# Kernel optimization log

Measured on AMD Instinct MI355X. Metric: run time of the kernel, lower is better.

The kernel has to match this reference:

```python
import jax, jax.numpy as jnp
import numpy as np

N_HEADS = 16
D_EMBED = 1024
N_CROSS = 768
D_HEAD = D_EMBED // N_HEADS


def setup_inputs() -> dict:
    key = jax.random.key(0)
    ks = jax.random.split(key, 10)
    B, S = 2, 2048
    x = jax.random.normal(ks[0], (B, S, D_EMBED), dtype=jnp.float32)
    context = jax.random.normal(ks[1], (B, S, N_CROSS), dtype=jnp.float32)
    sq = 1.0 / np.sqrt(D_EMBED)
    sc = 1.0 / np.sqrt(N_CROSS)
    Wq = jax.random.normal(ks[2], (D_EMBED, D_EMBED), dtype=jnp.float32) * sq
    bq = jnp.zeros((D_EMBED,), dtype=jnp.float32)
    Wk = jax.random.normal(ks[3], (N_CROSS, D_EMBED), dtype=jnp.float32) * sc
    bk = jnp.zeros((D_EMBED,), dtype=jnp.float32)
    Wv = jax.random.normal(ks[4], (N_CROSS, D_EMBED), dtype=jnp.float32) * sc
    bv = jnp.zeros((D_EMBED,), dtype=jnp.float32)
    Wo = jax.random.normal(ks[5], (D_EMBED, D_EMBED), dtype=jnp.float32) * sq
    bo = jnp.zeros((D_EMBED,), dtype=jnp.float32)
    return {"x": x, "context": context, "Wq": Wq, "bq": bq, "Wk": Wk, "bk": bk,
            "Wv": Wv, "bv": bv, "Wo": Wo, "bo": bo}


def reference(x, context, Wq, bq, Wk, bk, Wv, bv, Wo, bo):
    B, S, _ = x.shape

    def split_heads(t):  # [B,S,E] -> [B,H,S,Dh]
        return t.reshape(B, S, N_HEADS, D_HEAD).transpose(0, 2, 1, 3)

    q = split_heads(x @ Wq + bq)
    k = split_heads(context @ Wk + bk)
    v = split_heads(context @ Wv + bv)

    scale = 1.0 / np.sqrt(D_HEAD)
    scores = jnp.einsum('bhqd,bhkd->bhqk', q, k) * scale
    attn = jax.nn.softmax(scores, axis=-1)
    out = jnp.einsum('bhqk,bhkd->bhqd', attn, v)
    out = out.transpose(0, 2, 1, 3).reshape(B, S, D_EMBED)
    return out @ Wo + bo
```

## Files before the change

### kernel.cpp

```cpp
#include <hip/hip_runtime.h>
#include <math.h>


namespace {

typedef short bfr __attribute__((ext_vector_type(8)));
typedef short s4v __attribute__((ext_vector_type(4)));
typedef unsigned u4v __attribute__((ext_vector_type(4)));
typedef float accf __attribute__((ext_vector_type(16)));

#define MFMA32(a, b, c) __builtin_amdgcn_mfma_f32_32x32x16_bf16(a, b, c, 0, 0, 0)

__device__ inline short f2bf(float f) {
    unsigned u = __float_as_uint(f);
    u += 0x7fffu + ((u >> 16) & 1u);
    return (short)(u >> 16);
}
__device__ inline float bf2f(short s) {
    return __uint_as_float(((unsigned)(unsigned short)s) << 16);
}
__device__ inline float fexp2(float x) { return __builtin_amdgcn_exp2f(x); }
__device__ inline accf zero16() {
    accf z;
#pragma unroll
    for (int i = 0; i < 16; ++i) z[i] = 0.f;
    return z;
}
__device__ inline void dma16(const void* g, void* l) {
    __builtin_amdgcn_global_load_lds(
        (const __attribute__((address_space(1))) void*)g,
        (__attribute__((address_space(3))) void*)l, 16, 0, 0);
}

__global__ __launch_bounds__(256) void prep(
    const float* __restrict__ x, const float* __restrict__ ctx,
    short* __restrict__ xb, short* __restrict__ cb,
    const float* __restrict__ Wq, const float* __restrict__ Wk,
    const float* __restrict__ Wv, const float* __restrict__ Wo,
    short* __restrict__ Wqt, short* __restrict__ Wkt,
    short* __restrict__ Wvt, short* __restrict__ Wot) {
    __shared__ short t[64][68];
    const int bx = blockIdx.x;
    if (bx < 7168) {
        int i = bx * 256 + threadIdx.x;
        if (i < 1048576) {
            float4 v = ((const float4*)x)[i];
            s4v p = {f2bf(v.x), f2bf(v.y), f2bf(v.z), f2bf(v.w)};
            ((s4v*)xb)[i] = p;
        } else {
            int j = i - 1048576;
            float4 v = ((const float4*)ctx)[j];
            s4v p = {f2bf(v.x), f2bf(v.y), f2bf(v.z), f2bf(v.w)};
            ((s4v*)cb)[j] = p;
        }
        return;
    }
    const int idx = bx - 7168;
    const int z = idx >> 8, gy = (idx >> 4) & 15, gx = idx & 15;
    const float* W;
    short* Wt;
    int K;
    switch (z) {
        case 0: W = Wq; Wt = Wqt; K = 1024; break;
        case 1: W = Wk; Wt = Wkt; K = 768; break;
        case 2: W = Wv; Wt = Wvt; K = 768; break;
        default: W = Wo; Wt = Wot; K = 1024; break;
    }
    const int k0 = gy * 64;
    if (k0 >= K) return;
    const int tid = threadIdx.x;
    const int n0 = gx * 64;
    const int kr = tid >> 4, nc = (tid & 15) * 4;
#pragma unroll
    for (int rep = 0; rep < 4; ++rep) {
        int k = kr + rep * 16;
        float4 v = *(const float4*)&W[(size_t)(k0 + k) * 1024 + n0 + nc];
        t[nc + 0][k] = f2bf(v.x);
        t[nc + 1][k] = f2bf(v.y);
        t[nc + 2][k] = f2bf(v.z);
        t[nc + 3][k] = f2bf(v.w);
    }
    __syncthreads();
    const int nr = tid >> 4, kc = (tid & 15) * 4;
#pragma unroll
    for (int rep = 0; rep < 4; ++rep) {
        int n = nr + rep * 16;
        s4v p = {t[n][kc], t[n][kc + 1], t[n][kc + 2], t[n][kc + 3]};
        *(s4v*)&Wt[(size_t)(n0 + n) * K + k0 + kc] = p;
    }
}

__global__ __launch_bounds__(256) void gemm_qkv(
    const short* __restrict__ xb, const short* __restrict__ cb,
    const short* __restrict__ Wqt, const short* __restrict__ Wkt,
    const short* __restrict__ Wvt, const float* __restrict__ bq,
    const float* __restrict__ bk, const float* __restrict__ bv,
    short* __restrict__ Qf, short* __restrict__ Kf, short* __restrict__ Vt,
    float qscale) {
    const int z = blockIdx.z;
    const short* A  = (z == 0) ? xb : cb;
    const short* Bt = (z == 0) ? Wqt : ((z == 1) ? Wkt : Wvt);
    const float* bias = (z == 0) ? bq : ((z == 1) ? bk : bv);
    const int K = (z == 0) ? 1024 : 768;
    const float scale = (z == 0) ? qscale : 1.f;
    short* out = (z == 0) ? Qf : ((z == 1) ? Kf : Vt);

    __shared__ short As[4096];
    __shared__ short Bs[4096];
    const int t = threadIdx.x, lane = t & 63, w = t >> 6;
    const int lm = lane & 31, h2 = lane >> 5;
    const int wm = w & 1, wn = w >> 1;
    const int m0 = blockIdx.y * 128, n0 = blockIdx.x * 128;

    const int srow = t >> 2, scol = (t & 3) * 8;
    const short* ga = A + (size_t)(m0 + srow) * K + scol;
    const short* gb = Bt + (size_t)(n0 + srow) * K + scol;
    short* lA = As + w * 512;
    short* lB = Bs + w * 512;

    const int aoff = (wm * 64 + lm) * 32 + h2 * 8;
    const int boff = (wn * 64 + lm) * 32 + h2 * 8;

    accf acc[2][2] = {zero16(), zero16(), zero16(), zero16()};

    for (int kt = 0; kt < K; kt += 32) {
        __syncthreads();
        dma16(ga + kt, lA);
        dma16(ga + (size_t)64 * K + kt, lA + 2048);
        dma16(gb + kt, lB);
        dma16(gb + (size_t)64 * K + kt, lB + 2048);
        __syncthreads();
#pragma unroll
        for (int kk = 0; kk < 32; kk += 16) {
            bfr a0 = *(const bfr*)&As[aoff + kk];
            bfr a1 = *(const bfr*)&As[aoff + 1024 + kk];
            bfr b0 = *(const bfr*)&Bs[boff + kk];
            bfr b1 = *(const bfr*)&Bs[boff + 1024 + kk];
            acc[0][0] = MFMA32(a0, b0, acc[0][0]);
            acc[0][1] = MFMA32(a0, b1, acc[0][1]);
            acc[1][0] = MFMA32(a1, b0, acc[1][0]);
            acc[1][1] = MFMA32(a1, b1, acc[1][1]);
        }
    }

#pragma unroll
    for (int nt = 0; nt < 2; ++nt) {
        const int n = n0 + wn * 64 + nt * 32 + lm;
        const float bn = bias[n];
        const int hh = n >> 6, dd = n & 63;
#pragma unroll
        for (int mt = 0; mt < 2; ++mt) {
            const int mbase = m0 + wm * 64 + mt * 32 + 4 * h2;
            if (z != 2) {
                const int cb2 = (dd >> 4) * 512 + ((dd >> 3) & 1) * 256 + (dd & 7);
#pragma unroll
                for (int r = 0; r < 16; ++r) {
                    const int m = mbase + (r & 3) + 8 * (r >> 2);
                    const int bb = m >> 11, q = m & 2047;
                    float v = (acc[mt][nt][r] + bn) * scale;
                    out[((size_t)((bb * 16 + hh) * 64 + (q >> 5))) * 2048 +
                        cb2 + (q & 31) * 8] = f2bf(v);
                }
            } else {
                const int dblk = dd >> 5, lmv = dd & 31;
#pragma unroll
                for (int g = 0; g < 4; ++g) {
                    const int m = mbase + 8 * g;
                    const int bb = m >> 11, s = m & 2047;
                    const int kvt = s >> 6, kc = (s >> 4) & 3;
                    const int h2v = (s >> 3) & 1, j0 = s & 7;
                    s4v p = {f2bf(acc[mt][nt][4 * g + 0] + bn),
                             f2bf(acc[mt][nt][4 * g + 1] + bn),
                             f2bf(acc[mt][nt][4 * g + 2] + bn),
                             f2bf(acc[mt][nt][4 * g + 3] + bn)};
                    *(s4v*)(out +
                            ((size_t)(((bb * 16 + hh) * 32 + kvt) * 2 + dblk)) * 2048 +
                            kc * 512 + h2v * 256 + lmv * 8 + j0) = p;
                }
            }
        }
    }
}

__global__ __launch_bounds__(512) void gemm_out(
    const short* __restrict__ A, const short* __restrict__ Bt,
    const float* __restrict__ bias, float* __restrict__ out, int K) {
    __shared__ short As[4096];
    __shared__ short Bs[4096];
    const int t = threadIdx.x, lane = t & 63, w = t >> 6;
    const int lm = lane & 31, h2 = lane >> 5;
    const int wm = w & 1, wn = w >> 1;
    const int m0 = blockIdx.y * 128, n0 = blockIdx.x * 128;

    const int srow = t >> 2, scol = (t & 3) * 8;
    const short* ga = A + (size_t)(m0 + srow) * K + scol;
    const short* gb = Bt + (size_t)(n0 + srow) * K + scol;
    short* lA = As + w * 512;
    short* lB = Bs + w * 512;

    const int aoff = (wm * 64 + lm) * 32 + h2 * 8;
    const int boff = (wn * 32 + lm) * 32 + h2 * 8;

    accf acc[2] = {zero16(), zero16()};

    for (int kt = 0; kt < K; kt += 32) {
        __syncthreads();
        dma16(ga + kt, lA);
        dma16(gb + kt, lB);
        __syncthreads();
#pragma unroll
        for (int kk = 0; kk < 32; kk += 16) {
            bfr a0 = *(const bfr*)&As[aoff + kk];
            bfr a1 = *(const bfr*)&As[aoff + 1024 + kk];
            bfr b0 = *(const bfr*)&Bs[boff + kk];
            acc[0] = MFMA32(a0, b0, acc[0]);
            acc[1] = MFMA32(a1, b0, acc[1]);
        }
    }

    const int n = n0 + wn * 32 + lm;
    const float bn = bias[n];
#pragma unroll
    for (int mt = 0; mt < 2; ++mt) {
        const int mbase = m0 + wm * 64 + mt * 32 + 4 * h2;
#pragma unroll
        for (int r = 0; r < 16; ++r) {
            const int m = mbase + (r & 3) + 8 * (r >> 2);
            out[(size_t)m * 1024 + n] = acc[mt][r] + bn;
        }
    }
}

__global__ __launch_bounds__(256, 3) void attn(
    const short* __restrict__ Qf, const short* __restrict__ Kf,
    const short* __restrict__ Vt, short* __restrict__ part,
    float* __restrict__ lsum) {
    __shared__ short smem[16384];
    const int bid = blockIdx.x;
    const int hidx = bid & 31, qs = bid >> 5;
    const int split = qs & 1, qb = qs >> 1;
    const int b = hidx >> 4, h = hidx & 15;
    const int lane = threadIdx.x & 63, wv = threadIdx.x >> 6;
    const int lm = lane & 31, h2 = lane >> 5;
    const bool hb = h2 != 0;
    const int q0 = qb * 128 + wv * 32;

    const short* qbase =
        Qf + ((size_t)(hidx * 64 + (q0 >> 5))) * 2048 + lane * 8;
    bfr qf[4];
#pragma unroll
    for (int kc = 0; kc < 4; ++kc) qf[kc] = *(const bfr*)(qbase + kc * 512);

    const short* khead = Kf + (size_t)hidx * 131072 + split * 65536;
    const short* vhead = Vt + (size_t)hidx * 131072 + split * 65536;
    const short* gsrc =
        ((wv < 2) ? (khead + wv * 2048) : (vhead + (wv - 2) * 2048)) + lane * 8;

#pragma unroll
    for (int i = 0; i < 4; ++i)
        dma16(gsrc + i * 512, &smem[wv * 2048 + i * 512]);

    accf oa0 = zero16(), oa1 = zero16();
    float la0 = 0.f, la1 = 0.f;

#pragma unroll 1
    for (int it = 0; it < 16; ++it) {
        const int p = it & 1;
        __syncthreads();
        if (it + 1 < 16) {
            const short* gn = gsrc + (size_t)(it + 1) * 4096;
            short* ln = &smem[(1 - p) * 8192 + wv * 2048];
#pragma unroll
            for (int i = 0; i < 4; ++i) dma16(gn + i * 512, ln + i * 512);
        }
        const short* kb = &smem[p * 8192];
        bfr kf0[4], kf1[4], vf0[4], vf1[4];
#pragma unroll
        for (int kc = 0; kc < 4; ++kc) {
            kf0[kc] = *(const bfr*)&kb[kc * 512 + lane * 8];
            kf1[kc] = *(const bfr*)&kb[2048 + kc * 512 + lane * 8];
            vf0[kc] = *(const bfr*)&kb[4096 + kc * 512 + lane * 8];
            vf1[kc] = *(const bfr*)&kb[6144 + kc * 512 + lane * 8];
        }
        accf s0 = zero16(), s1 = zero16();
#pragma unroll
        for (int kc = 0; kc < 4; ++kc) {
            s0 = MFMA32(kf0[kc], qf[kc], s0);
            s1 = MFMA32(kf1[kc], qf[kc], s1);
        }

#pragma unroll
        for (int i = 0; i < 16; ++i) s0[i] = fexp2(s0[i]);
#pragma unroll
        for (int i = 0; i < 16; ++i) s1[i] = fexp2(s1[i]);
#pragma unroll
        for (int i = 0; i < 16; ++i) {
            if (i & 1) la1 += s0[i] + s1[i];
            else       la0 += s0[i] + s1[i];
        }

        bfr pb[4];
#pragma unroll
        for (int kc = 0; kc < 4; ++kc) {
            const accf& s = (kc < 2) ? s0 : s1;
            const int base = 8 * (kc & 1);
            unsigned Lw0 = __builtin_amdgcn_perm(__float_as_uint(s[base + 1]),
                                                 __float_as_uint(s[base + 0]),
                                                 0x07060302u);
            unsigned Lw1 = __builtin_amdgcn_perm(__float_as_uint(s[base + 3]),
                                                 __float_as_uint(s[base + 2]),
                                                 0x07060302u);
            unsigned Hw0 = __builtin_amdgcn_perm(__float_as_uint(s[base + 5]),
                                                 __float_as_uint(s[base + 4]),
                                                 0x07060302u);
            unsigned Hw1 = __builtin_amdgcn_perm(__float_as_uint(s[base + 7]),
                                                 __float_as_uint(s[base + 6]),
                                                 0x07060302u);
            unsigned c0 = hb ? Lw0 : Hw0;
            unsigned c1 = hb ? Lw1 : Hw1;
            unsigned r0 = (unsigned)__shfl_xor((int)c0, 32);
            unsigned r1 = (unsigned)__shfl_xor((int)c1, 32);
            u4v pw = {hb ? r0 : Lw0, hb ? r1 : Lw1,
                      hb ? Hw0 : r0, hb ? Hw1 : r1};
            pb[kc] = __builtin_bit_cast(bfr, pw);
        }

#pragma unroll
        for (int kc = 0; kc < 4; ++kc) {
            oa0 = MFMA32(vf0[kc], pb[kc], oa0);
            oa1 = MFMA32(vf1[kc], pb[kc], oa1);
        }
    }

    float ls = la0 + la1;
    ls += __shfl_xor(ls, 32);
    if (!hb) lsum[((size_t)(split * 2 + b) * 16 + h) * 2048 + q0 + lm] = ls;

    short* orow = part + (size_t)split * 4194304 +
                  (size_t)(b * 2048 + q0 + lm) * 1024 + h * 64;
#pragma unroll
    for (int dt = 0; dt < 2; ++dt) {
        const accf& oa = dt ? oa1 : oa0;
#pragma unroll
        for (int g = 0; g < 4; ++g) {
            const int d0 = dt * 32 + 4 * h2 + 8 * g;
            s4v p = {f2bf(oa[4 * g + 0]), f2bf(oa[4 * g + 1]),
                     f2bf(oa[4 * g + 2]), f2bf(oa[4 * g + 3])};
            *(s4v*)(orow + d0) = p;
        }
    }
}

__global__ __launch_bounds__(256) void combine(
    const short* __restrict__ p0, const short* __restrict__ p1,
    const float* __restrict__ lsum, short* __restrict__ ao) {
    const int t = blockIdx.x * 256 + threadIdx.x;
    const int col8 = t & 127, m = t >> 7;
    const int h = col8 >> 3;
    const int b = m >> 11, q = m & 2047;
    const float l0 = lsum[((size_t)(0 + b) * 16 + h) * 2048 + q];
    const float l1 = lsum[((size_t)(2 + b) * 16 + h) * 2048 + q];
    const float inv = 1.f / (l0 + l1);
    const size_t e0 = (size_t)m * 1024 + col8 * 8;
    bfr a = *(const bfr*)(p0 + e0);
    bfr c = *(const bfr*)(p1 + e0);
    bfr r;
#pragma unroll
    for (int j = 0; j < 8; ++j) r[j] = f2bf((bf2f(a[j]) + bf2f(c[j])) * inv);
    *(bfr*)(ao + e0) = r;
}

}

extern "C" void kernel_launch(void* const* d_in, const int* in_sizes, int n_in,
                              void* d_out, int out_size, void* d_ws,
                              size_t ws_size, hipStream_t stream) {
    const float* x   = (const float*)d_in[0];
    const float* ctx = (const float*)d_in[1];
    const float* Wq  = (const float*)d_in[2];
    const float* bq  = (const float*)d_in[3];
    const float* Wk  = (const float*)d_in[4];
    const float* bk  = (const float*)d_in[5];
    const float* Wv  = (const float*)d_in[6];
    const float* bv  = (const float*)d_in[7];
    const float* Wo  = (const float*)d_in[8];
    const float* bo  = (const float*)d_in[9];

    short* xb  = (short*)d_ws;
    short* cb  = xb + (size_t)4096 * 1024;
    short* Wqt = cb + (size_t)4096 * 768;
    short* Wkt = Wqt + (size_t)1024 * 1024;
    short* Wvt = Wkt + (size_t)1024 * 768;
    short* Wot = Wvt + (size_t)1024 * 768;
    short* Qf  = Wot + (size_t)1024 * 1024;
    short* Kf  = Qf + (size_t)4096 * 1024;
    short* Vt  = Kf + (size_t)4096 * 1024;
    short* p0  = Vt + (size_t)4096 * 1024;
    short* p1  = p0 + (size_t)4096 * 1024;
    float* lsum = (float*)(p1 + (size_t)4096 * 1024);

    prep<<<8192, 256, 0, stream>>>(x, ctx, xb, cb, Wq, Wk, Wv, Wo,
                                   Wqt, Wkt, Wvt, Wot);

    const float qscale = 0.125f * 1.44269504088896f;
    gemm_qkv<<<dim3(8, 32, 3), 256, 0, stream>>>(xb, cb, Wqt, Wkt, Wvt,
                                                 bq, bk, bv, Qf, Kf, Vt,
                                                 qscale);

    attn<<<1024, 256, 0, stream>>>(Qf, Kf, Vt, p0, lsum);
    combine<<<2048, 256, 0, stream>>>(p0, p1, lsum, xb);

    gemm_out<<<dim3(8, 32), 512, 0, stream>>>(xb, Wot, bo, (float*)d_out, 1024);
}
```

Baseline: 222.9 us.

## Double-buffer LDS tiles and XOR-swizzle layout in projection GEMMs

Both projection GEMMs now use two LDS buffers per operand. The next K-tile is prefetched into the idle buffer while MFMAs run on the current one, so each iteration needs one barrier instead of two. The LDS tile layout is also XOR-swizzled on the store side and unswizzled on the reads, to avoid bank conflicts on the row-strided fragment loads. The cost is twice the shared memory per block, which may lower occupancy. Correctness depends on dma16 completing before the next barrier.

After: 216.9 us. -2.7%, faster.

```diff
diff --git a/kernel.cpp b/kernel.cpp
--- a/kernel.cpp
+++ b/kernel.cpp
@@ -102,40 +102,53 @@
     const short* Bt = (z == 0) ? Wqt : ((z == 1) ? Wkt : Wvt);
     const float* bias = (z == 0) ? bq : ((z == 1) ? bk : bv);
     const int K = (z == 0) ? 1024 : 768;
+    const int NIT = K / 32;
     const float scale = (z == 0) ? qscale : 1.f;
     short* out = (z == 0) ? Qf : ((z == 1) ? Kf : Vt);
 
-    __shared__ short As[4096];
-    __shared__ short Bs[4096];
+    __shared__ short As[8192];
+    __shared__ short Bs[8192];
     const int t = threadIdx.x, lane = t & 63, w = t >> 6;
     const int lm = lane & 31, h2 = lane >> 5;
     const int wm = w & 1, wn = w >> 1;
     const int m0 = blockIdx.y * 128, n0 = blockIdx.x * 128;
 
-    const int srow = t >> 2, scol = (t & 3) * 8;
+    const int st = t ^ ((t >> 3) & 7);
+    const int srow = st >> 2, scol = (st & 3) * 8;
     const short* ga = A + (size_t)(m0 + srow) * K + scol;
     const short* gb = Bt + (size_t)(n0 + srow) * K + scol;
-    short* lA = As + w * 512;
-    short* lB = Bs + w * 512;
-
-    const int aoff = (wm * 64 + lm) * 32 + h2 * 8;
-    const int boff = (wn * 64 + lm) * 32 + h2 * 8;
+
+    const int xorv = (lm >> 1) & 7;
+    const int rA0 = wm * 64 + lm, rB0 = wn * 64 + lm;
 
     accf acc[2][2] = {zero16(), zero16(), zero16(), zero16()};
 
-    for (int kt = 0; kt < K; kt += 32) {
+    dma16(ga, &As[w * 512]);
+    dma16(ga + (size_t)64 * K, &As[2048 + w * 512]);
+    dma16(gb, &Bs[w * 512]);
+    dma16(gb + (size_t)64 * K, &Bs[2048 + w * 512]);
+
+#pragma unroll 1
+    for (int it = 0; it < NIT; ++it) {
+        const int p = it & 1;
         __syncthreads();
-        dma16(ga + kt, lA);
-        dma16(ga + (size_t)64 * K + kt, lA + 2048);
-        dma16(gb + kt, lB);
-        dma16(gb + (size_t)64 * K + kt, lB + 2048);
-        __syncthreads();
-#pragma unroll
-        for (int kk = 0; kk < 32; kk += 16) {
-            bfr a0 = *(const bfr*)&As[aoff + kk];
-            bfr a1 = *(const bfr*)&As[aoff + 1024 + kk];
-            bfr b0 = *(const bfr*)&Bs[boff + kk];
-            bfr b1 = *(const bfr*)&Bs[boff + 1024 + kk];
+        if (it + 1 < NIT) {
+            const int kt = (it + 1) * 32;
+            short* lA = &As[(1 - p) * 4096 + w * 512];
+            short* lB = &Bs[(1 - p) * 4096 + w * 512];
+            dma16(ga + kt, lA);
+            dma16(ga + (size_t)64 * K + kt, lA + 2048);
+            dma16(gb + kt, lB);
+            dma16(gb + (size_t)64 * K + kt, lB + 2048);
+        }
+        const short* bA = &As[p * 4096];
+        const short* bB = &Bs[p * 4096];
+#pragma unroll
+        for (int kk8 = 0; kk8 < 4; kk8 += 2) {
+            bfr a0 = *(const bfr*)&bA[((rA0 * 4 + h2 + kk8) ^ xorv) * 8];
+            bfr a1 = *(const bfr*)&bA[(((rA0 + 32) * 4 + h2 + kk8) ^ xorv) * 8];
+            bfr b0 = *(const bfr*)&bB[((rB0 * 4 + h2 + kk8) ^ xorv) * 8];
+            bfr b1 = *(const bfr*)&bB[(((rB0 + 32) * 4 + h2 + kk8) ^ xorv) * 8];
             acc[0][0] = MFMA32(a0, b0, acc[0][0]);
             acc[0][1] = MFMA32(a0, b1, acc[0][1]);
             acc[1][0] = MFMA32(a1, b0, acc[1][0]);
@@ -185,34 +198,43 @@
 __global__ __launch_bounds__(512) void gemm_out(
     const short* __restrict__ A, const short* __restrict__ Bt,
     const float* __restrict__ bias, float* __restrict__ out, int K) {
-    __shared__ short As[4096];
-    __shared__ short Bs[4096];
+    __shared__ short As[8192];
+    __shared__ short Bs[8192];
     const int t = threadIdx.x, lane = t & 63, w = t >> 6;
     const int lm = lane & 31, h2 = lane >> 5;
     const int wm = w & 1, wn = w >> 1;
     const int m0 = blockIdx.y * 128, n0 = blockIdx.x * 128;
-
-    const int srow = t >> 2, scol = (t & 3) * 8;
+    const int NIT = K / 32;
+
+    const int st = t ^ ((t >> 3) & 7);
+    const int srow = st >> 2, scol = (st & 3) * 8;
     const short* ga = A + (size_t)(m0 + srow) * K + scol;
     const short* gb = Bt + (size_t)(n0 + srow) * K + scol;
-    short* lA = As + w * 512;
-    short* lB = Bs + w * 512;
-
-    const int aoff = (wm * 64 + lm) * 32 + h2 * 8;
-    const int boff = (wn * 32 + lm) * 32 + h2 * 8;
+
+    const int xorv = (lm >> 1) & 7;
+    const int rA0 = wm * 64 + lm, rB0 = wn * 32 + lm;
 
     accf acc[2] = {zero16(), zero16()};
 
-    for (int kt = 0; kt < K; kt += 32) {
+    dma16(ga, &As[w * 512]);
+    dma16(gb, &Bs[w * 512]);
+
+#pragma unroll 1
+    for (int it = 0; it < NIT; ++it) {
+        const int p = it & 1;
         __syncthreads();
-        dma16(ga + kt, lA);
-        dma16(gb + kt, lB);
-        __syncthreads();
-#pragma unroll
-        for (int kk = 0; kk < 32; kk += 16) {
-            bfr a0 = *(const bfr*)&As[aoff + kk];
-            bfr a1 = *(const bfr*)&As[aoff + 1024 + kk];
-            bfr b0 = *(const bfr*)&Bs[boff + kk];
+        if (it + 1 < NIT) {
+            const int kt = (it + 1) * 32;
+            dma16(ga + kt, &As[(1 - p) * 4096 + w * 512]);
+            dma16(gb + kt, &Bs[(1 - p) * 4096 + w * 512]);
+        }
+        const short* bA = &As[p * 4096];
+        const short* bB = &Bs[p * 4096];
+#pragma unroll
+        for (int kk8 = 0; kk8 < 4; kk8 += 2) {
+            bfr a0 = *(const bfr*)&bA[((rA0 * 4 + h2 + kk8) ^ xorv) * 8];
+            bfr a1 = *(const bfr*)&bA[(((rA0 + 32) * 4 + h2 + kk8) ^ xorv) * 8];
+            bfr b0 = *(const bfr*)&bB[((rB0 * 4 + h2 + kk8) ^ xorv) * 8];
             acc[0] = MFMA32(a0, b0, acc[0]);
             acc[1] = MFMA32(a1, b0, acc[1]);
         }
```
